# Performance work log

Hardware: AMD Instinct MI355X
Metric: run time of the kernel (lower is better)

## Reference

```python
import jax, jax.numpy as jnp
import numpy as np

D_MODEL = 256; N_HEADS = 8; N_LEVELS = 4; N_POINTS = 4
D_HEAD = D_MODEL // N_HEADS


def setup_inputs() -> dict:
    key = jax.random.key(0)
    ks = jax.random.split(key, 8)
    N, Lq = 4, 4096
    shapes = np.array([4096, 2048, 1024, 512], dtype=np.int32)  # temporal lengths per level
    Len_in = int(shapes.sum())  # 7680
    start = np.concatenate([[0], np.cumsum(shapes)[:-1]]).astype(np.int32)
    HLP = N_HEADS * N_LEVELS * N_POINTS
    return {
        "query": jax.random.normal(ks[0], (N, Lq, D_MODEL), jnp.float32),
        "reference_points": jax.random.uniform(ks[1], (N, Lq, N_LEVELS, 1), jnp.float32),
        "input_flatten": jax.random.normal(ks[2], (N, Len_in, D_MODEL), jnp.float32),
        "input_spatial_shapes": jnp.asarray(shapes),
        "input_level_start_index": jnp.asarray(start),
        "W_off": jax.random.normal(ks[3], (D_MODEL, HLP), jnp.float32) * 0.01,
        "b_off": jax.random.normal(ks[4], (HLP,), jnp.float32) * 2.0,
        "W_aw": jax.random.normal(ks[5], (D_MODEL, HLP), jnp.float32) * 0.02,
        "b_aw": jnp.zeros((HLP,), jnp.float32),
        "W_v": jax.random.normal(ks[6], (D_MODEL, D_MODEL), jnp.float32) / np.sqrt(D_MODEL).astype(np.float32),
        "b_v": jnp.zeros((D_MODEL,), jnp.float32),
        "W_out": jax.random.normal(ks[7], (D_MODEL, D_MODEL), jnp.float32) / np.sqrt(D_MODEL).astype(np.float32),
        "b_out": jnp.zeros((D_MODEL,), jnp.float32),
    }


def reference(query, reference_points, input_flatten, input_spatial_shapes,
              input_level_start_index, W_off, b_off, W_aw, b_aw, W_v, b_v,
              W_out, b_out):
    N, Lq, C = query.shape
    M, L, P, Dh = N_HEADS, N_LEVELS, N_POINTS, D_HEAD
    S = input_flatten.shape[1]

    value = (input_flatten @ W_v + b_v).reshape(N, S, M, Dh)
    off = (query @ W_off + b_off).reshape(N, Lq, M, L, P)
    aw = jax.nn.softmax((query @ W_aw + b_aw).reshape(N, Lq, M, L * P), axis=-1)
    aw = aw.reshape(N, Lq, M, L, P)

    # reference_points last dim == 1 branch: loc = ref + off / T_l, in [0,1]
    T = input_spatial_shapes.astype(jnp.float32)[None, None, None, :, None]  # [1,1,1,L,1]
    loc = reference_points[:, :, None, :, None, 0] + off / T  # [N,Lq,M,L,P]

    # grid_sample(align_corners=False, padding_mode='border') along W with H=1, y=0.5:
    # pixel coord x = loc*T - 0.5, clamped to [0, T-1], then linear interp.
    x = jnp.clip(loc * T - 0.5, 0.0, T - 1.0)
    x0 = jnp.floor(x)
    w1 = x - x0                                   # frac weight for right neighbor
    i0 = x0.astype(jnp.int32)
    i1 = jnp.minimum(i0 + 1, input_spatial_shapes[None, None, None, :, None] - 1)
    base = input_level_start_index[None, None, None, :, None]
    g0 = i0 + base                                # global flattened indices [N,Lq,M,L,P]
    g1 = i1 + base

    v = value.transpose(0, 2, 1, 3)               # [N,M,S,Dh]

    def gather(idx):
        idxt = idx.transpose(0, 2, 1, 3, 4).reshape(N, M, Lq * L * P, 1)
        return jnp.take_along_axis(v, idxt, axis=2).reshape(N, M, Lq, L, P, Dh)

    s0 = gather(g0)
    s1 = gather(g1)
    w1t = w1.transpose(0, 2, 1, 3, 4)[..., None]   # [N,M,Lq,L,P,1]
    samp = s0 * (1.0 - w1t) + s1 * w1t             # [N,M,Lq,L,P,Dh]

    awt = aw.transpose(0, 2, 1, 3, 4)[..., None]
    out = (samp * awt).sum(axis=(3, 4))            # [N,M,Lq,Dh]
    out = out.transpose(0, 2, 1, 3).reshape(N, Lq, M * Dh)
    return out @ W_out + b_out
```

## Files before the change

### kernel.cpp

```cpp
#include <hip/hip_runtime.h>
#include <hip/hip_bf16.h>
#include <cstddef>
#include <cstdint>

#define D_MODEL   256
#define N_HEADS   8
#define N_LEVELS  4
#define N_POINTS  4
#define D_HEAD    32
#define HLP       128
#define NBATCH    4
#define LQ        4096
#define S_LEN     7680

typedef __attribute__((ext_vector_type(8))) short  short8;
typedef __attribute__((ext_vector_type(4))) float  f32x4;
typedef __attribute__((ext_vector_type(8))) unsigned short ushort8;

__device__ __forceinline__ unsigned short f2bf(float x) {
    __hip_bfloat16 h = __float2bfloat16(x);
    return *reinterpret_cast<unsigned short*>(&h);
}
__device__ __forceinline__ float bf2f(unsigned short u) {
    unsigned int v = ((unsigned int)u) << 16;
    return *reinterpret_cast<float*>(&v);
}

__device__ __forceinline__ void gload_lds16(const void* g, void* l) {
    __builtin_amdgcn_global_load_lds(
        (const __attribute__((address_space(1))) void*)g,
        (__attribute__((address_space(3))) void*)l,
        16, 0, 0);
}

__global__ __launch_bounds__(256) void prep_kernel(
    const float* __restrict__ W_v,  const float* __restrict__ W_off,
    const float* __restrict__ W_aw, const float* __restrict__ W_out,
    const float* __restrict__ b_off, const float* __restrict__ b_aw,
    unsigned short* __restrict__ Wv_t, unsigned short* __restrict__ Wcat_t,
    unsigned short* __restrict__ Wout_t, float* __restrict__ bcat)
{
    __shared__ float t[64][65];
    const int z   = blockIdx.z;
    const int k0  = blockIdx.y * 64;
    const int n0  = blockIdx.x * 64;
    const int tid = threadIdx.x;

    const float* src; int srcN; int cs; unsigned short* dst;
    if (z == 0)      { src = W_v;   srcN = 256; cs = n0;       dst = Wv_t;  }
    else if (z == 2) { src = W_out; srcN = 256; cs = n0;       dst = Wout_t;}
    else if (n0 < 128){ src = W_off; srcN = 128; cs = n0;      dst = Wcat_t;}
    else             { src = W_aw;  srcN = 128; cs = n0 - 128; dst = Wcat_t;}

    #pragma unroll
    for (int i = 0; i < 16; ++i) {
        int idx = tid + i * 256;
        int kk = idx >> 6, nn = idx & 63;
        t[kk][nn] = src[(size_t)(k0 + kk) * srcN + cs + nn];
    }
    __syncthreads();
    #pragma unroll
    for (int i = 0; i < 16; ++i) {
        int idx = tid + i * 256;
        int nn = idx >> 6, kk = idx & 63;
        dst[(size_t)(n0 + nn) * 256 + k0 + kk] = f2bf(t[kk][nn]);
    }
    if (z == 1 && blockIdx.x == 0 && blockIdx.y == 0) {
        bcat[tid] = (tid < 128) ? b_off[tid] : b_aw[tid - 128];
    }
}

__global__ __launch_bounds__(256) void gemm_vp_kernel(
    const float* __restrict__ inflat, const float* __restrict__ query,
    const unsigned short* __restrict__ Wv_t, const unsigned short* __restrict__ Wcat_t,
    const float* __restrict__ b_v, const float* __restrict__ bcat,
    unsigned short* __restrict__ value2, float* __restrict__ P)
{
    __shared__ alignas(16) unsigned short Als[8][64][8];
    __shared__ alignas(16) unsigned short Bls[8][64][8];

    const int job = blockIdx.x;
    const bool is_val = (job < 480);
    const int jj   = is_val ? job : (job - 480);
    const int row0 = (jj >> 1) * 128;
    const int col0 = (jj & 1) * 128;
    const float* A = is_val ? inflat : query;
    const unsigned short* Bt = is_val ? Wv_t : Wcat_t;
    const float* bias = is_val ? b_v : bcat;

    const int tid  = threadIdx.x;
    const int lane = tid & 63;
    const int w    = tid >> 6;
    const int wm   = w & 1;
    const int wn   = w >> 1;
    const int lr   = lane & 15;
    const int lk   = (lane >> 4) * 8;

    f32x4 acc[4][4] = {};

    for (int kt = 0; kt < 8; ++kt) {
        const int k0 = kt * 32;
        #pragma unroll
        for (int c = 0; c < 2; ++c) {
            const int im = w * 2 + c;
            const float* ap = A + (size_t)(row0 + im * 16 + lr) * 256 + k0 + lk;
            const float4 a0 = *(const float4*)(ap);
            const float4 a1 = *(const float4*)(ap + 4);
            short8 pk;
            pk[0] = (short)f2bf(a0.x); pk[1] = (short)f2bf(a0.y);
            pk[2] = (short)f2bf(a0.z); pk[3] = (short)f2bf(a0.w);
            pk[4] = (short)f2bf(a1.x); pk[5] = (short)f2bf(a1.y);
            pk[6] = (short)f2bf(a1.z); pk[7] = (short)f2bf(a1.w);
            *(short8*)&Als[im][lane][0] = pk;
            const size_t gb = (size_t)(col0 + im * 16 + lr) * 256 + k0 + lk;
            gload_lds16(Bt + gb, &Bls[im][0][0]);
        }
        __syncthreads();

        short8 af[4], bfr[4];
        #pragma unroll
        for (int i = 0; i < 4; ++i) af[i]  = *(const short8*)&Als[wm * 4 + i][lane][0];
        #pragma unroll
        for (int j = 0; j < 4; ++j) bfr[j] = *(const short8*)&Bls[wn * 4 + j][lane][0];

        #pragma unroll
        for (int i = 0; i < 4; ++i)
            #pragma unroll
            for (int j = 0; j < 4; ++j)
                acc[i][j] = __builtin_amdgcn_mfma_f32_16x16x32_bf16(
                    af[i], bfr[j], acc[i][j], 0, 0, 0);
        __syncthreads();
    }

    const int prow = (lane >> 4) * 4;
    const int pcol = lane & 15;
    if (is_val) {
        const int n  = row0 / S_LEN;
        const int s0 = row0 - n * S_LEN;
        const int gg = col0 >> 7;
        unsigned short* dst = value2 + ((size_t)(n * 2 + gg) * S_LEN + s0) * 128;
        #pragma unroll
        for (int j = 0; j < 4; ++j) {
            const int inner = wn * 64 + j * 16 + pcol;
            const float bs = bias[col0 + inner];
            #pragma unroll
            for (int i = 0; i < 4; ++i) {
                #pragma unroll
                for (int r = 0; r < 4; ++r) {
                    const int rl = wm * 64 + i * 16 + prow + r;
                    dst[(size_t)rl * 128 + inner] = f2bf(acc[i][j][r] + bs);
                }
            }
        }
    } else {
        #pragma unroll
        for (int j = 0; j < 4; ++j) {
            const int col = col0 + wn * 64 + j * 16 + pcol;
            const float bs = bias[col];
            #pragma unroll
            for (int i = 0; i < 4; ++i) {
                #pragma unroll
                for (int r = 0; r < 4; ++r) {
                    const int row = row0 + wm * 64 + i * 16 + prow + r;
                    P[(size_t)row * 256 + col] = acc[i][j][r] + bs;
                }
            }
        }
    }
}

__global__ __launch_bounds__(256) void gemm_out_kernel(
    const unsigned short* __restrict__ A,
    const unsigned short* __restrict__ Bt,
    const float* __restrict__ bias,
    float* __restrict__ Cout)
{
    __shared__ alignas(16) unsigned short Als[8][64][8];
    __shared__ alignas(16) unsigned short Bls[8][64][8];

    const int tid  = threadIdx.x;
    const int lane = tid & 63;
    const int w    = tid >> 6;
    const int wm   = w & 1;
    const int wn   = w >> 1;
    const int row0 = blockIdx.y * 128;
    const int col0 = blockIdx.x * 128;
    const int lr   = lane & 15;
    const int lk   = (lane >> 4) * 8;

    f32x4 acc[4][4] = {};

    for (int kt = 0; kt < 8; ++kt) {
        const int k0 = kt * 32;
        #pragma unroll
        for (int c = 0; c < 2; ++c) {
            const int im = w * 2 + c;
            gload_lds16(A + (size_t)(row0 + im * 16 + lr) * 256 + k0 + lk, &Als[im][0][0]);
            gload_lds16(Bt + (size_t)(col0 + im * 16 + lr) * 256 + k0 + lk, &Bls[im][0][0]);
        }
        __syncthreads();

        short8 af[4], bfr[4];
        #pragma unroll
        for (int i = 0; i < 4; ++i) af[i]  = *(const short8*)&Als[wm * 4 + i][lane][0];
        #pragma unroll
        for (int j = 0; j < 4; ++j) bfr[j] = *(const short8*)&Bls[wn * 4 + j][lane][0];

        #pragma unroll
        for (int i = 0; i < 4; ++i)
            #pragma unroll
            for (int j = 0; j < 4; ++j)
                acc[i][j] = __builtin_amdgcn_mfma_f32_16x16x32_bf16(
                    af[i], bfr[j], acc[i][j], 0, 0, 0);
        __syncthreads();
    }

    const int prow = (lane >> 4) * 4;
    const int pcol = lane & 15;
    #pragma unroll
    for (int j = 0; j < 4; ++j) {
        const int col = col0 + wn * 64 + j * 16 + pcol;
        const float bs = bias[col];
        #pragma unroll
        for (int i = 0; i < 4; ++i) {
            #pragma unroll
            for (int r = 0; r < 4; ++r) {
                const int row = row0 + wm * 64 + i * 16 + prow + r;
                Cout[(size_t)row * 256 + col] = acc[i][j][r] + bs;
            }
        }
    }
}

__global__ __launch_bounds__(256) void sample_kernel(
    const float* __restrict__ P, const float* __restrict__ refp,
    const int* __restrict__ shapes, const int* __restrict__ lstart,
    const unsigned short* __restrict__ value2, unsigned short* __restrict__ tout)
{
    __shared__ int   sG0[16][65];
    __shared__ int   sG1[16][65];
    __shared__ float sW [16][65];
    __shared__ float sA [16][65];

    const int b   = blockIdx.x;
    const int xcd = b & 7;
    const int n   = xcd >> 1;
    const int g   = xcd & 1;
    const int q0  = (b >> 3) * 16;
    const int nq0 = n * LQ + q0;
    const int tid = threadIdx.x;

    #pragma unroll
    for (int it = 0; it < 4; ++it) {
        const int idx = tid + it * 256;
        const int q   = idx >> 6;
        const int jl  = idx & 63;
        const int l   = (jl >> 2) & 3;
        const int jg  = g * 64 + jl;
        const int nq  = nq0 + q;
        const float off   = __builtin_nontemporal_load(P + (size_t)nq * 256 + jg);
        const float logit = __builtin_nontemporal_load(P + (size_t)nq * 256 + 128 + jg);
        const float ref   = __builtin_nontemporal_load(refp + (size_t)nq * N_LEVELS + l);
        const int   sh    = shapes[l];
        const float T     = (float)sh;
        float x = ref * T + off - 0.5f;
        x = fminf(fmaxf(x, 0.0f), T - 1.0f);
        const float x0 = floorf(x);
        const int   i0 = (int)x0;
        const int   i1 = min(i0 + 1, sh - 1);
        const int   base = lstart[l];
        sG0[q][jl] = i0 + base;
        sG1[q][jl] = i1 + base;
        sW [q][jl] = x - x0;
        sA [q][jl] = logit;
    }
    __syncthreads();

    if (tid < 64) {
        const int q  = tid >> 2;
        const int mh = tid & 3;
        float e[16];
        float mx = -1e30f;
        #pragma unroll
        for (int i = 0; i < 16; ++i) { e[i] = sA[q][mh * 16 + i]; mx = fmaxf(mx, e[i]); }
        float s = 0.f;
        #pragma unroll
        for (int i = 0; i < 16; ++i) { e[i] = __expf(e[i] - mx); s += e[i]; }
        const float rs = 1.0f / s;
        #pragma unroll
        for (int i = 0; i < 16; ++i) sA[q][mh * 16 + i] = e[i] * rs;
    }
    __syncthreads();

    const int q  = tid >> 4;
    const int r  = tid & 15;
    const int mh = r >> 2;
    const int ql = r & 3;
    const unsigned short* vb =
        value2 + (size_t)xcd * S_LEN * 128 + mh * 32 + ql * 8;

    float acc[8] = {};
    #pragma unroll
    for (int i = 0; i < 16; ++i) {
        const int j = mh * 16 + i;
        const float a  = sA[q][j];
        const float ww = sW[q][j];
        const ushort8 u0 = *(const ushort8*)(vb + (size_t)sG0[q][j] * 128);
        const ushort8 u1 = *(const ushort8*)(vb + (size_t)sG1[q][j] * 128);
        #pragma unroll
        for (int d = 0; d < 8; ++d) {
            const float v0 = bf2f(u0[d]);
            const float v1 = bf2f(u1[d]);
            acc[d] += a * (v0 + ww * (v1 - v0));
        }
    }
    ushort8 o;
    #pragma unroll
    for (int d = 0; d < 8; ++d) o[d] = f2bf(acc[d]);
    __builtin_nontemporal_store(o,
        (ushort8*)(tout + (size_t)(nq0 + q) * 256 + g * 128 + mh * 32 + ql * 8));
}

extern "C" void kernel_launch(void* const* d_in, const int* in_sizes, int n_in,
                              void* d_out, int out_size, void* d_ws, size_t ws_size,
                              hipStream_t stream)
{
    const float* query  = (const float*)d_in[0];
    const float* refp   = (const float*)d_in[1];
    const float* inflat = (const float*)d_in[2];
    const int*   shapes = (const int*)d_in[3];
    const int*   lstart = (const int*)d_in[4];
    const float* W_off  = (const float*)d_in[5];
    const float* b_off  = (const float*)d_in[6];
    const float* W_aw   = (const float*)d_in[7];
    const float* b_aw   = (const float*)d_in[8];
    const float* W_v    = (const float*)d_in[9];
    const float* b_v    = (const float*)d_in[10];
    const float* W_out  = (const float*)d_in[11];
    const float* b_out  = (const float*)d_in[12];

    const int M_val = NBATCH * S_LEN;
    const int M_q   = NBATCH * LQ;

    char* p = (char*)d_ws;
    unsigned short* value2 = (unsigned short*)p; p += (size_t)M_val * D_MODEL * 2;
    float*          P      = (float*)p;          p += (size_t)M_q * 256 * 4;
    unsigned short* tbuf   = (unsigned short*)p; p += (size_t)M_q * D_MODEL * 2;
    unsigned short* Wv_t   = (unsigned short*)p; p += 256 * 256 * 2;
    unsigned short* Wcat_t = (unsigned short*)p; p += 256 * 256 * 2;
    unsigned short* Wout_t = (unsigned short*)p; p += 256 * 256 * 2;
    float*          bcat   = (float*)p;          p += 256 * 4;

    prep_kernel<<<dim3(4, 4, 3), 256, 0, stream>>>(
        W_v, W_off, W_aw, W_out, b_off, b_aw, Wv_t, Wcat_t, Wout_t, bcat);
    gemm_vp_kernel<<<736, 256, 0, stream>>>(
        inflat, query, Wv_t, Wcat_t, b_v, bcat, value2, P);
    sample_kernel<<<2048, 256, 0, stream>>>(
        P, refp, shapes, lstart, value2, tbuf);
    gemm_out_kernel<<<dim3(2, M_q / 128), 256, 0, stream>>>(
        tbuf, Wout_t, b_out, (float*)d_out);
}
```

Before: 162.2 us.

## Fuse sampling with output projection and store value per head

The separate sampling and output-GEMM kernels are merged into one kernel. Each block handles 8 queries across all heads, writes the sampled result to a padded 16-row LDS tile, and runs MFMA against W_out read straight from global memory. The value tensor is re-laid out as [batch, head, S, 32] so each head's gather lands in a contiguous region. The i1 index is now computed on the fly. This removes the tbuf round trip and a launch, but half of each MFMA tile is zero padding and each block re-reads all of W_out from global/L2.

```diff
diff --git a/kernel.cpp b/kernel.cpp
--- a/kernel.cpp
+++ b/kernel.cpp
@@ -12,6 +12,7 @@
 #define NBATCH    4
 #define LQ        4096
 #define S_LEN     7680
+#define QB        8
 
 typedef __attribute__((ext_vector_type(8))) short  short8;
 typedef __attribute__((ext_vector_type(4))) float  f32x4;
@@ -74,7 +75,7 @@
     const float* __restrict__ inflat, const float* __restrict__ query,
     const unsigned short* __restrict__ Wv_t, const unsigned short* __restrict__ Wcat_t,
     const float* __restrict__ b_v, const float* __restrict__ bcat,
-    unsigned short* __restrict__ value2, float* __restrict__ P)
+    unsigned short* __restrict__ value3, float* __restrict__ P)
 {
     __shared__ alignas(16) unsigned short Als[8][64][8];
     __shared__ alignas(16) unsigned short Bls[8][64][8];
@@ -137,18 +138,18 @@
     if (is_val) {
         const int n  = row0 / S_LEN;
         const int s0 = row0 - n * S_LEN;
-        const int gg = col0 >> 7;
-        unsigned short* dst = value2 + ((size_t)(n * 2 + gg) * S_LEN + s0) * 128;
         #pragma unroll
         for (int j = 0; j < 4; ++j) {
-            const int inner = wn * 64 + j * 16 + pcol;
-            const float bs = bias[col0 + inner];
+            const int col = col0 + wn * 64 + j * 16 + pcol;
+            const float bs = bias[col];
+            const int m = col >> 5, d = col & 31;
+            unsigned short* dst = value3 + ((size_t)(n * 8 + m) * S_LEN + s0) * 32 + d;
             #pragma unroll
             for (int i = 0; i < 4; ++i) {
                 #pragma unroll
                 for (int r = 0; r < 4; ++r) {
                     const int rl = wm * 64 + i * 16 + prow + r;
-                    dst[(size_t)rl * 128 + inner] = f2bf(acc[i][j][r] + bs);
+                    dst[(size_t)rl * 32] = f2bf(acc[i][j][r] + bs);
                 }
             }
         }
@@ -169,156 +170,134 @@
     }
 }
 
-__global__ __launch_bounds__(256) void gemm_out_kernel(
-    const unsigned short* __restrict__ A,
-    const unsigned short* __restrict__ Bt,
-    const float* __restrict__ bias,
-    float* __restrict__ Cout)
-{
-    __shared__ alignas(16) unsigned short Als[8][64][8];
-    __shared__ alignas(16) unsigned short Bls[8][64][8];
-
-    const int tid  = threadIdx.x;
-    const int lane = tid & 63;
-    const int w    = tid >> 6;
-    const int wm   = w & 1;
-    const int wn   = w >> 1;
-    const int row0 = blockIdx.y * 128;
-    const int col0 = blockIdx.x * 128;
-    const int lr   = lane & 15;
-    const int lk   = (lane >> 4) * 8;
-
-    f32x4 acc[4][4] = {};
-
-    for (int kt = 0; kt < 8; ++kt) {
-        const int k0 = kt * 32;
-        #pragma unroll
-        for (int c = 0; c < 2; ++c) {
-            const int im = w * 2 + c;
-            gload_lds16(A + (size_t)(row0 + im * 16 + lr) * 256 + k0 + lk, &Als[im][0][0]);
-            gload_lds16(Bt + (size_t)(col0 + im * 16 + lr) * 256 + k0 + lk, &Bls[im][0][0]);
-        }
-        __syncthreads();
-
-        short8 af[4], bfr[4];
-        #pragma unroll
-        for (int i = 0; i < 4; ++i) af[i]  = *(const short8*)&Als[wm * 4 + i][lane][0];
-        #pragma unroll
-        for (int j = 0; j < 4; ++j) bfr[j] = *(const short8*)&Bls[wn * 4 + j][lane][0];
-
-        #pragma unroll
-        for (int i = 0; i < 4; ++i)
-            #pragma unroll
-            for (int j = 0; j < 4; ++j)
-                acc[i][j] = __builtin_amdgcn_mfma_f32_16x16x32_bf16(
-                    af[i], bfr[j], acc[i][j], 0, 0, 0);
-        __syncthreads();
-    }
-
-    const int prow = (lane >> 4) * 4;
-    const int pcol = lane & 15;
-    #pragma unroll
-    for (int j = 0; j < 4; ++j) {
-        const int col = col0 + wn * 64 + j * 16 + pcol;
-        const float bs = bias[col];
-        #pragma unroll
-        for (int i = 0; i < 4; ++i) {
-            #pragma unroll
-            for (int r = 0; r < 4; ++r) {
-                const int row = row0 + wm * 64 + i * 16 + prow + r;
-                Cout[(size_t)row * 256 + col] = acc[i][j][r] + bs;
-            }
-        }
-    }
-}
-
-__global__ __launch_bounds__(256) void sample_kernel(
+__global__ __launch_bounds__(256) void sample_out_kernel(
     const float* __restrict__ P, const float* __restrict__ refp,
     const int* __restrict__ shapes, const int* __restrict__ lstart,
-    const unsigned short* __restrict__ value2, unsigned short* __restrict__ tout)
+    const unsigned short* __restrict__ value3,
+    const unsigned short* __restrict__ Wout_t,
+    const float* __restrict__ b_out,
+    float* __restrict__ out)
 {
-    __shared__ int   sG0[16][65];
-    __shared__ int   sG1[16][65];
-    __shared__ float sW [16][65];
-    __shared__ float sA [16][65];
-
-    const int b   = blockIdx.x;
-    const int xcd = b & 7;
-    const int n   = xcd >> 1;
-    const int g   = xcd & 1;
-    const int q0  = (b >> 3) * 16;
-    const int nq0 = n * LQ + q0;
-    const int tid = threadIdx.x;
+    __shared__ int   sG0[QB][132];
+    __shared__ float sW [QB][132];
+    __shared__ float sA [QB][132];
+    __shared__ alignas(16) unsigned short T[16][264];
+    __shared__ int glim[4];
+
+    const int b    = blockIdx.x;
+    const int xcd  = b & 7;
+    const int n    = xcd >> 1;
+    const int half = xcd & 1;
+    const int slot = b >> 3;
+    const int q0   = (slot * 2 + half) * QB;
+    const int nq0  = n * LQ + q0;
+    const int tid  = threadIdx.x;
+
+    if (tid < 4) glim[tid] = lstart[tid] + shapes[tid] - 1;
 
     #pragma unroll
     for (int it = 0; it < 4; ++it) {
         const int idx = tid + it * 256;
-        const int q   = idx >> 6;
-        const int jl  = idx & 63;
-        const int l   = (jl >> 2) & 3;
-        const int jg  = g * 64 + jl;
+        const int q   = idx >> 7;
+        const int j   = idx & 127;
+        const int l   = (j >> 2) & 3;
         const int nq  = nq0 + q;
-        const float off   = __builtin_nontemporal_load(P + (size_t)nq * 256 + jg);
-        const float logit = __builtin_nontemporal_load(P + (size_t)nq * 256 + 128 + jg);
+        const float off   = __builtin_nontemporal_load(P + (size_t)nq * 256 + j);
+        const float logit = __builtin_nontemporal_load(P + (size_t)nq * 256 + 128 + j);
         const float ref   = __builtin_nontemporal_load(refp + (size_t)nq * N_LEVELS + l);
         const int   sh    = shapes[l];
-        const float T     = (float)sh;
-        float x = ref * T + off - 0.5f;
-        x = fminf(fmaxf(x, 0.0f), T - 1.0f);
+        const float Tf    = (float)sh;
+        float x = ref * Tf + off - 0.5f;
+        x = fminf(fmaxf(x, 0.0f), Tf - 1.0f);
         const float x0 = floorf(x);
-        const int   i0 = (int)x0;
-        const int   i1 = min(i0 + 1, sh - 1);
-        const int   base = lstart[l];
-        sG0[q][jl] = i0 + base;
-        sG1[q][jl] = i1 + base;
-        sW [q][jl] = x - x0;
-        sA [q][jl] = logit;
+        sG0[q][j] = (int)x0 + lstart[l];
+        sW [q][j] = x - x0;
+        sA [q][j] = logit;
     }
     __syncthreads();
 
     if (tid < 64) {
-        const int q  = tid >> 2;
-        const int mh = tid & 3;
+        const int q = tid >> 3;
+        const int m = tid & 7;
         float e[16];
         float mx = -1e30f;
         #pragma unroll
-        for (int i = 0; i < 16; ++i) { e[i] = sA[q][mh * 16 + i]; mx = fmaxf(mx, e[i]); }
+        for (int i = 0; i < 16; ++i) { e[i] = sA[q][m * 16 + i]; mx = fmaxf(mx, e[i]); }
         float s = 0.f;
         #pragma unroll
         for (int i = 0; i < 16; ++i) { e[i] = __expf(e[i] - mx); s += e[i]; }
         const float rs = 1.0f / s;
         #pragma unroll
-        for (int i = 0; i < 16; ++i) sA[q][mh * 16 + i] = e[i] * rs;
+        for (int i = 0; i < 16; ++i) sA[q][m * 16 + i] = e[i] * rs;
+    }
+    {
+        const int zr = 8 + (tid >> 5);
+        const int zc = (tid & 31) * 8;
+        *(ushort8*)&T[zr][zc] = (ushort8)0;
     }
     __syncthreads();
 
-    const int q  = tid >> 4;
-    const int r  = tid & 15;
-    const int mh = r >> 2;
-    const int ql = r & 3;
-    const unsigned short* vb =
-        value2 + (size_t)xcd * S_LEN * 128 + mh * 32 + ql * 8;
-
-    float acc[8] = {};
-    #pragma unroll
-    for (int i = 0; i < 16; ++i) {
-        const int j = mh * 16 + i;
-        const float a  = sA[q][j];
-        const float ww = sW[q][j];
-        const ushort8 u0 = *(const ushort8*)(vb + (size_t)sG0[q][j] * 128);
-        const ushort8 u1 = *(const ushort8*)(vb + (size_t)sG1[q][j] * 128);
-        #pragma unroll
-        for (int d = 0; d < 8; ++d) {
-            const float v0 = bf2f(u0[d]);
-            const float v1 = bf2f(u1[d]);
-            acc[d] += a * (v0 + ww * (v1 - v0));
-        }
-    }
-    ushort8 o;
-    #pragma unroll
-    for (int d = 0; d < 8; ++d) o[d] = f2bf(acc[d]);
-    __builtin_nontemporal_store(o,
-        (ushort8*)(tout + (size_t)(nq0 + q) * 256 + g * 128 + mh * 32 + ql * 8));
+    {
+        const int q  = tid >> 5;
+        const int r  = tid & 31;
+        const int m  = r >> 2;
+        const int ql = r & 3;
+        const unsigned short* vb =
+            value3 + (size_t)(n * 8 + m) * S_LEN * 32 + ql * 8;
+
+        float acc[8] = {};
+        #pragma unroll
+        for (int i = 0; i < 16; ++i) {
+            const int j = m * 16 + i;
+            const float a  = sA[q][j];
+            const float ww = sW[q][j];
+            const int g0 = sG0[q][j];
+            const int g1 = min(g0 + 1, glim[i >> 2]);
+            const ushort8 u0 = *(const ushort8*)(vb + (size_t)g0 * 32);
+            const ushort8 u1 = *(const ushort8*)(vb + (size_t)g1 * 32);
+            #pragma unroll
+            for (int d = 0; d < 8; ++d) {
+                const float v0 = bf2f(u0[d]);
+                const float v1 = bf2f(u1[d]);
+                acc[d] += a * (v0 + ww * (v1 - v0));
+            }
+        }
+        ushort8 o;
+        #pragma unroll
+        for (int d = 0; d < 8; ++d) o[d] = f2bf(acc[d]);
+        *(ushort8*)&T[q][m * 32 + ql * 8] = o;
+    }
+    __syncthreads();
+
+    {
+        const int w    = tid >> 6;
+        const int lane = tid & 63;
+        const int lr   = lane & 15;
+        const int lk   = (lane >> 4) * 8;
+        f32x4 acc4[4] = {};
+        for (int kt = 0; kt < 8; ++kt) {
+            const short8 af = *(const short8*)&T[lr][kt * 32 + lk];
+            #pragma unroll
+            for (int j = 0; j < 4; ++j) {
+                const int col = w * 64 + j * 16 + lr;
+                const short8 bf = *(const short8*)(Wout_t + (size_t)col * 256 + kt * 32 + lk);
+                acc4[j] = __builtin_amdgcn_mfma_f32_16x16x32_bf16(af, bf, acc4[j], 0, 0, 0);
+            }
+        }
+        const int prow = (lane >> 4) * 4;
+        if (prow < 8) {
+            #pragma unroll
+            for (int j = 0; j < 4; ++j) {
+                const int col = w * 64 + j * 16 + lr;
+                const float bs = b_out[col];
+                #pragma unroll
+                for (int r = 0; r < 4; ++r) {
+                    const int row = prow + r;
+                    out[(size_t)(nq0 + row) * 256 + col] = acc4[j][r] + bs;
+                }
+            }
+        }
+    }
 }
 
 extern "C" void kernel_launch(void* const* d_in, const int* in_sizes, int n_in,
@@ -343,9 +322,8 @@
     const int M_q   = NBATCH * LQ;
 
     char* p = (char*)d_ws;
-    unsigned short* value2 = (unsigned short*)p; p += (size_t)M_val * D_MODEL * 2;
+    unsigned short* value3 = (unsigned short*)p; p += (size_t)M_val * D_MODEL * 2;
     float*          P      = (float*)p;          p += (size_t)M_q * 256 * 4;
-    unsigned short* tbuf   = (unsigned short*)p; p += (size_t)M_q * D_MODEL * 2;
     unsigned short* Wv_t   = (unsigned short*)p; p += 256 * 256 * 2;
     unsigned short* Wcat_t = (unsigned short*)p; p += 256 * 256 * 2;
     unsigned short* Wout_t = (unsigned short*)p; p += 256 * 256 * 2;
@@ -354,9 +332,7 @@
     prep_kernel<<<dim3(4, 4, 3), 256, 0, stream>>>(
         W_v, W_off, W_aw, W_out, b_off, b_aw, Wv_t, Wcat_t, Wout_t, bcat);
     gemm_vp_kernel<<<736, 256, 0, stream>>>(
-        inflat, query, Wv_t, Wcat_t, b_v, bcat, value2, P);
-    sample_kernel<<<2048, 256, 0, stream>>>(
-        P, refp, shapes, lstart, value2, tbuf);
-    gemm_out_kernel<<<dim3(2, M_q / 128), 256, 0, stream>>>(
-        tbuf, Wout_t, b_out, (float*)d_out);
-}
+        inflat, query, Wv_t, Wcat_t, b_v, bcat, value3, P);
+    sample_out_kernel<<<2048, 256, 0, stream>>>(
+        P, refp, shapes, lstart, value3, Wout_t, b_out, (float*)d_out);
+}
```

Measured after the change: 181.3 us. 1.12x slower.
